# Kernel tuning notes

Measured on AMD Instinct MI355X. Metric: run time of the kernel, lower is better.

## Reference

```python
import math
import jax, jax.numpy as jnp
import numpy as np

N, T, D, H, DH = 4, 2048, 1024, 16, 64
CAP = 30.0
EPS = 1e-5


def _layernorm(x, g, b):
    m = jnp.mean(x, axis=-1, keepdims=True)
    v = jnp.mean(jnp.square(x - m), axis=-1, keepdims=True)
    return (x - m) * jax.lax.rsqrt(v + EPS) * g + b


def _rope(x):
    # x: [N, H, t, d]; interleaved rotary (rotary-embedding-torch style), theta=10000
    t, d = x.shape[2], x.shape[3]
    inv_freq = 1.0 / (10000.0 ** (jnp.arange(0, d, 2, dtype=jnp.float32) / d))
    ang = jnp.arange(t, dtype=jnp.float32)[:, None] * inv_freq[None, :]  # [t, d/2]
    cos, sin = jnp.cos(ang), jnp.sin(ang)
    x1, x2 = x[..., 0::2], x[..., 1::2]
    r1 = x1 * cos - x2 * sin
    r2 = x1 * sin + x2 * cos
    return jnp.stack([r1, r2], axis=-1).reshape(x.shape)


def setup_inputs() -> dict:
    key = jax.random.key(0)
    ks = jax.random.split(key, 8)
    s = 0.02
    lengths = jax.random.randint(ks[6], (N,), T // 2, T + 1).astype(jnp.int32)
    key_padding_mask = jnp.arange(T)[None, :] >= lengths[:, None]  # True = pad
    attn_mask = jnp.triu(jnp.ones((T, T), dtype=bool), 1)  # causal: True = masked
    return {
        "x": jax.random.normal(ks[0], (N, T, D), jnp.float32),
        "ln_g": jnp.ones((D,), jnp.float32),
        "ln_b": jnp.zeros((D,), jnp.float32),
        "Wq": jax.random.normal(ks[1], (D, H * DH), jnp.float32) * s,
        "bq": jnp.zeros((H * DH,), jnp.float32),
        "Wk": jax.random.normal(ks[2], (D, H * DH), jnp.float32) * s,
        "bk": jnp.zeros((H * DH,), jnp.float32),
        "Wv": jax.random.normal(ks[3], (D, H * DH), jnp.float32) * s,
        "bv": jnp.zeros((H * DH,), jnp.float32),
        "Wo": jax.random.normal(ks[4], (H * DH, D), jnp.float32) * s,
        "bo": jnp.zeros((D,), jnp.float32),
        "key_padding_mask": key_padding_mask,
        "attn_mask": attn_mask,
        "key_value_sequence_lengths": lengths,
    }


def reference(x, ln_g, ln_b, Wq, bq, Wk, bk, Wv, bv, Wo, bo,
              key_padding_mask, attn_mask, key_value_sequence_lengths):
    n, t, _ = x.shape
    h = _layernorm(x, ln_g, ln_b)  # shared LN for q/k/v (self-attention)
    q = (h @ Wq + bq).reshape(n, t, H, DH).transpose(0, 2, 1, 3)  # [n,H,t,d]
    k = (h @ Wk + bk).reshape(n, t, H, DH).transpose(0, 2, 1, 3)
    v = (h @ Wv + bv).reshape(n, t, H, DH).transpose(0, 2, 1, 3)
    q = _rope(q)
    k = _rope(k)
    scores = jnp.einsum('bhtd,bhTd->bhtT', q, k) / math.sqrt(DH)
    scores = CAP * jnp.tanh(scores / CAP)  # tanh soft-cap
    mask = key_padding_mask[:, None, None, :] | attn_mask[None, None, :, :]
    scores = jnp.where(mask, -jnp.inf, scores)
    attn = jax.nn.softmax(scores, axis=-1)
    out = jnp.einsum('bhtT,bhTd->bhtd', attn, v)
    out = out.transpose(0, 2, 1, 3).reshape(n, t, H * DH)
    return out @ Wo + bo
```

## Files before the change

### kernel.cpp

```cpp
#include <hip/hip_runtime.h>
#include <hip/hip_bf16.h>

typedef unsigned short u16;
typedef unsigned int   u32;
typedef __bf16 bf16x8 __attribute__((ext_vector_type(8)));
typedef float  f32x4  __attribute__((ext_vector_type(4)));

#define NB 4
#define T_ 2048
#define D_ 1024
#define H_ 16
#define DH 64
#define M_ (NB * T_)
#define PSTR 72

__device__ __forceinline__ float bf2f(u16 u) {
    union { u32 i; float f; } v; v.i = ((u32)u) << 16; return v.f;
}
__device__ __forceinline__ u16 f2bf(float f) {
    union { float fl; u32 i; } v; v.fl = f;
    u32 r = v.i + 0x7fff + ((v.i >> 16) & 1);
    return (u16)(r >> 16);
}

__device__ __forceinline__ void gl_lds16(const u16* g, u16* l) {
    __builtin_amdgcn_global_load_lds((const __attribute__((address_space(1))) void*)g,
                                     (__attribute__((address_space(3))) void*)l,
                                     16, 0, 0);
}

__device__ __forceinline__ int detect_f32(const u16* p) {
    int weird = 0;
    const int lane = threadIdx.x & 63;
    #pragma unroll
    for (int i = 0; i < 4; ++i) {
        const u16 u = p[lane * 4 + i];
        const int e = (u >> 7) & 0xFF;
        weird += (e == 0xFF || (e >= 0x01 && e <= 0x3F) || (e >= 0xC0 && e <= 0xFE));
    }
    #pragma unroll
    for (int off = 32; off; off >>= 1) weird += __shfl_xor(weird, off);
    return weird >= 16;
}

__device__ __forceinline__ int read_len(const void* raw, int b) {
    const int* a32 = (const int*)raw;
    bool ok32 = true;
    #pragma unroll
    for (int i = 0; i < NB; ++i) {
        const int v = a32[i];
        if (v < 1 || v > T_) ok32 = false;
    }
    int v = ok32 ? a32[b] : (int)((const long long*)raw)[b];
    return min(max(v, 1), T_);
}

__global__ __launch_bounds__(256) void ln_kernel(const void* __restrict__ xraw,
                                                 const void* __restrict__ graw,
                                                 const void* __restrict__ braw,
                                                 u16* __restrict__ h) {
    const int row = blockIdx.x;
    const int tid = threadIdx.x;
    const int isf = detect_f32((const u16*)xraw);

    float xv[4];
    if (isf) {
        const float* xr = (const float*)xraw + (size_t)row * D_;
        *(float4*)xv = *(const float4*)&xr[tid * 4];
    } else {
        const u16* xr = (const u16*)xraw + (size_t)row * D_;
        u16 loc[4] __attribute__((aligned(8)));
        *(uint2*)loc = *(const uint2*)&xr[tid * 4];
        #pragma unroll
        for (int i = 0; i < 4; ++i) xv[i] = bf2f(loc[i]);
    }

    float s = xv[0] + xv[1] + xv[2] + xv[3];
    float q = xv[0]*xv[0] + xv[1]*xv[1] + xv[2]*xv[2] + xv[3]*xv[3];

    #pragma unroll
    for (int off = 32; off; off >>= 1) {
        s += __shfl_xor(s, off);
        q += __shfl_xor(q, off);
    }
    __shared__ float red[8];
    const int wave = tid >> 6, lane = tid & 63;
    if (lane == 0) { red[wave] = s; red[4 + wave] = q; }
    __syncthreads();
    s = red[0] + red[1] + red[2] + red[3];
    q = red[4] + red[5] + red[6] + red[7];

    const float mean = s * (1.0f / D_);
    const float var  = q * (1.0f / D_) - mean * mean;
    const float rs   = rsqrtf(var + 1e-5f);

    u16 o[4] __attribute__((aligned(8)));
    #pragma unroll
    for (int i = 0; i < 4; ++i) {
        const int c = tid * 4 + i;
        const float gv = isf ? ((const float*)graw)[c] : bf2f(((const u16*)graw)[c]);
        const float bv = isf ? ((const float*)braw)[c] : bf2f(((const u16*)braw)[c]);
        o[i] = f2bf((xv[i] - mean) * rs * gv + bv);
    }
    *(uint2*)&h[(size_t)row * D_ + tid * 4] = *(uint2*)o;
}

__global__ __launch_bounds__(256) void wconv4_kernel(const void* __restrict__ W0,
                                                     const void* __restrict__ W1,
                                                     const void* __restrict__ W2,
                                                     const void* __restrict__ W3,
                                                     u16* __restrict__ Wt0,
                                                     u16* __restrict__ Wt1,
                                                     u16* __restrict__ Wt2,
                                                     u16* __restrict__ Wt3) {
    __shared__ u16 tile[64][PSTR];
    const int z = blockIdx.z;
    const void* Wraw = (z == 0) ? W0 : (z == 1) ? W1 : (z == 2) ? W2 : W3;
    u16* Wt          = (z == 0) ? Wt0 : (z == 1) ? Wt1 : (z == 2) ? Wt2 : Wt3;
    const int isf = detect_f32((const u16*)Wraw);
    const int n0 = blockIdx.x * 64;
    const int k0 = blockIdx.y * 64;
    const int tid = threadIdx.x;
    const int tr  = tid >> 2;
    const int tc  = (tid & 3) * 16;

    if (isf) {
        const float* W = (const float*)Wraw;
        #pragma unroll
        for (int i = 0; i < 16; ++i)
            tile[tc + i][tr] = f2bf(W[(size_t)(k0 + tr) * D_ + n0 + tc + i]);
    } else {
        const u16* W = (const u16*)Wraw;
        #pragma unroll
        for (int i = 0; i < 16; ++i)
            tile[tc + i][tr] = W[(size_t)(k0 + tr) * D_ + n0 + tc + i];
    }
    __syncthreads();
    *(uint4*)&Wt[(size_t)(n0 + tr) * D_ + k0 + tc]     = *(uint4*)&tile[tr][tc];
    *(uint4*)&Wt[(size_t)(n0 + tr) * D_ + k0 + tc + 8] = *(uint4*)&tile[tr][tc + 8];
}

__global__ __launch_bounds__(256) void wconv_kernel(const void* __restrict__ Wraw,
                                                    u16* __restrict__ Wt) {
    __shared__ u16 tile[64][PSTR];
    const int isf = detect_f32((const u16*)Wraw);
    const int n0 = blockIdx.x * 64;
    const int k0 = blockIdx.y * 64;
    const int tid = threadIdx.x;
    const int tr  = tid >> 2;
    const int tc  = (tid & 3) * 16;

    if (isf) {
        const float* W = (const float*)Wraw;
        #pragma unroll
        for (int i = 0; i < 16; ++i)
            tile[tc + i][tr] = f2bf(W[(size_t)(k0 + tr) * D_ + n0 + tc + i]);
    } else {
        const u16* W = (const u16*)Wraw;
        #pragma unroll
        for (int i = 0; i < 16; ++i)
            tile[tc + i][tr] = W[(size_t)(k0 + tr) * D_ + n0 + tc + i];
    }
    __syncthreads();
    *(uint4*)&Wt[(size_t)(n0 + tr) * D_ + k0 + tc]     = *(uint4*)&tile[tr][tc];
    *(uint4*)&Wt[(size_t)(n0 + tr) * D_ + k0 + tc + 8] = *(uint4*)&tile[tr][tc + 8];
}

__global__ __launch_bounds__(256) void rope_kernel(float2* __restrict__ tab) {
    const int gid = blockIdx.x * 256 + threadIdx.x;
    const int t = gid >> 5, i = gid & 31;
    const float inv = exp2f(-(float)i * 0.41524101186092f);
    const float ang = (float)t * inv;
    float sv, cv;
    sincosf(ang, &sv, &cv);
    tab[gid] = make_float2(cv, sv);
}

__global__ __launch_bounds__(256) void vtrans_kernel(const u16* __restrict__ vtmp,
                                                     u16* __restrict__ vt) {
    __shared__ u16 tile[64][PSTR];
    const int bh = blockIdx.y;
    const int b  = bh >> 4;
    const int hh = bh & 15;
    const int t0 = blockIdx.x * 64;
    const int tid = threadIdx.x;
    const int tr  = tid >> 2;
    const int tc  = (tid & 3) * 16;

    #pragma unroll
    for (int i = 0; i < 16; ++i)
        tile[tc + i][tr] = vtmp[(size_t)(b * T_ + t0 + tr) * D_ + hh * DH + tc + i];
    __syncthreads();
    u16* dst = vt + (size_t)bh * DH * T_ + (size_t)tr * T_ + t0;
    *(uint4*)&dst[tc]     = *(uint4*)&tile[tr][tc];
    *(uint4*)&dst[tc + 8] = *(uint4*)&tile[tr][tc + 8];
}

__global__ __launch_bounds__(256) void qkv_kernel(const u16* __restrict__ A,
                                                  const u16* __restrict__ Wt3,
                                                  const void* __restrict__ Braw,
                                                  const void* __restrict__ bqr,
                                                  const void* __restrict__ bkr,
                                                  const void* __restrict__ bvr,
                                                  u16* __restrict__ qo,
                                                  u16* __restrict__ ko,
                                                  u16* __restrict__ vo,
                                                  const float2* __restrict__ tab) {
    __shared__ __align__(16) u16 As[128 * 32];
    __shared__ __align__(16) u16 Bs[128 * 32];

    const int tid   = threadIdx.x;
    const int wave  = tid >> 6;
    const int lane  = tid & 63;
    const int quad  = lane >> 4;
    const int lr    = lane & 15;
    const int ntile = blockIdx.x * 128;
    const int mtile = blockIdx.y * 128;
    const int seg   = ntile >> 10;

    const int isf = detect_f32((const u16*)Braw);

    const int srow = wave * 32 + (lane >> 2);
    const int scol = (lane & 3) * 8;
    const u16* aptr0 = A   + (size_t)(mtile + srow) * D_ + scol;
    const u16* aptr1 = A   + (size_t)(mtile + srow + 16) * D_ + scol;
    const u16* bptr0 = Wt3 + (size_t)(ntile + srow) * D_ + scol;
    const u16* bptr1 = Wt3 + (size_t)(ntile + srow + 16) * D_ + scol;
    u16* alds0 = As + wave * 1024;
    u16* alds1 = As + wave * 1024 + 512;
    u16* blds0 = Bs + wave * 1024;
    u16* blds1 = Bs + wave * 1024 + 512;

    const int mbase = (wave >> 1) * 64;
    const int nbase = (wave & 1) * 64;

    f32x4 acc[4][4];
    #pragma unroll
    for (int m = 0; m < 4; ++m)
        #pragma unroll
        for (int n = 0; n < 4; ++n)
            acc[m][n] = (f32x4){0.f, 0.f, 0.f, 0.f};

    for (int k0 = 0; k0 < D_; k0 += 32) {
        gl_lds16(aptr0 + k0, alds0);
        gl_lds16(aptr1 + k0, alds1);
        gl_lds16(bptr0 + k0, blds0);
        gl_lds16(bptr1 + k0, blds1);
        __syncthreads();

        bf16x8 af[4], bfr[4];
        #pragma unroll
        for (int m = 0; m < 4; ++m)
            af[m] = *(const bf16x8*)&As[(mbase + m * 16 + lr) * 32 + quad * 8];
        #pragma unroll
        for (int n = 0; n < 4; ++n)
            bfr[n] = *(const bf16x8*)&Bs[(nbase + n * 16 + lr) * 32 + quad * 8];
        #pragma unroll
        for (int m = 0; m < 4; ++m)
            #pragma unroll
            for (int n = 0; n < 4; ++n)
                acc[m][n] = __builtin_amdgcn_mfma_f32_16x16x32_bf16(af[m], bfr[n], acc[m][n], 0, 0, 0);

        __syncthreads();
    }

    const void* biasraw = (seg == 0) ? bqr : (seg == 1) ? bkr : bvr;
    u16* out            = (seg == 0) ? qo  : (seg == 1) ? ko  : vo;
    const int nloc = (ntile & 1023) + nbase;

    #pragma unroll
    for (int m = 0; m < 4; ++m) {
        #pragma unroll
        for (int n = 0; n < 4; ++n) {
            const int ncl = nloc + n * 16 + lr;
            const float bv = isf ? ((const float*)biasraw)[ncl]
                                 : bf2f(((const u16*)biasraw)[ncl]);
            #pragma unroll
            for (int r = 0; r < 4; ++r) {
                const int mrow = mtile + mbase + m * 16 + quad * 4 + r;
                float v = acc[m][n][r] + bv;
                if (seg < 2) {
                    const float other = __shfl_xor(v, 1);
                    const int d = ncl & (DH - 1);
                    const int t = mrow & (T_ - 1);
                    const float2 cs = tab[t * 32 + (d >> 1)];
                    v = (d & 1) ? (other * cs.y + v * cs.x) : (v * cs.x - other * cs.y);
                }
                out[(size_t)mrow * D_ + ncl] = f2bf(v);
            }
        }
    }
}

__global__ __launch_bounds__(256) void gemm128_kernel(const u16* __restrict__ A,
                                                      const u16* __restrict__ Bt,
                                                      const void* __restrict__ Braw,
                                                      const void* __restrict__ biasraw,
                                                      void* __restrict__ out,
                                                      const int mode) {
    __shared__ __align__(16) u16 As[128 * 32];
    __shared__ __align__(16) u16 Bs[128 * 32];

    const int tid   = threadIdx.x;
    const int wave  = tid >> 6;
    const int lane  = tid & 63;
    const int quad  = lane >> 4;
    const int lr    = lane & 15;
    const int ntile = blockIdx.x * 128;
    const int mtile = blockIdx.y * 128;

    const int isf = detect_f32((const u16*)Braw);

    const int srow = wave * 32 + (lane >> 2);
    const int scol = (lane & 3) * 8;
    const u16* aptr0 = A  + (size_t)(mtile + srow) * D_ + scol;
    const u16* aptr1 = A  + (size_t)(mtile + srow + 16) * D_ + scol;
    const u16* bptr0 = Bt + (size_t)(ntile + srow) * D_ + scol;
    const u16* bptr1 = Bt + (size_t)(ntile + srow + 16) * D_ + scol;
    u16* alds0 = As + wave * 1024;
    u16* alds1 = As + wave * 1024 + 512;
    u16* blds0 = Bs + wave * 1024;
    u16* blds1 = Bs + wave * 1024 + 512;

    const int mbase = (wave >> 1) * 64;
    const int nbase = (wave & 1) * 64;

    f32x4 acc[4][4];
    #pragma unroll
    for (int m = 0; m < 4; ++m)
        #pragma unroll
        for (int n = 0; n < 4; ++n)
            acc[m][n] = (f32x4){0.f, 0.f, 0.f, 0.f};

    for (int k0 = 0; k0 < D_; k0 += 32) {
        gl_lds16(aptr0 + k0, alds0);
        gl_lds16(aptr1 + k0, alds1);
        gl_lds16(bptr0 + k0, blds0);
        gl_lds16(bptr1 + k0, blds1);
        __syncthreads();

        bf16x8 af[4], bfr[4];
        #pragma unroll
        for (int m = 0; m < 4; ++m)
            af[m] = *(const bf16x8*)&As[(mbase + m * 16 + lr) * 32 + quad * 8];
        #pragma unroll
        for (int n = 0; n < 4; ++n)
            bfr[n] = *(const bf16x8*)&Bs[(nbase + n * 16 + lr) * 32 + quad * 8];
        #pragma unroll
        for (int m = 0; m < 4; ++m)
            #pragma unroll
            for (int n = 0; n < 4; ++n)
                acc[m][n] = __builtin_amdgcn_mfma_f32_16x16x32_bf16(af[m], bfr[n], acc[m][n], 0, 0, 0);

        __syncthreads();
    }

    #pragma unroll
    for (int m = 0; m < 4; ++m) {
        #pragma unroll
        for (int n = 0; n < 4; ++n) {
            const int ncol = ntile + nbase + n * 16 + lr;
            const float bv = isf ? ((const float*)biasraw)[ncol]
                                 : bf2f(((const u16*)biasraw)[ncol]);
            #pragma unroll
            for (int r = 0; r < 4; ++r) {
                const int mrow = mtile + mbase + m * 16 + quad * 4 + r;
                float v = acc[m][n][r] + bv;
                if (mode == 2) {
                    const float other = __shfl_xor(v, 1);
                    const int d = ncol & (DH - 1);
                    const int t = mrow & (T_ - 1);
                    const int i = d >> 1;
                    const float inv = exp2f(-(float)i * 0.41524101186092f);
                    const float ang = (float)t * inv;
                    float sv, cv;
                    __sincosf(ang, &sv, &cv);
                    v = (d & 1) ? (other * sv + v * cv) : (v * cv - other * sv);
                }
                const int d  = ncol & (DH - 1);
                const int hh = ncol >> 6;
                const int t  = mrow & (T_ - 1);
                const int bb = mrow >> 11;
                if (mode == 0) {
                    if (isf) ((float*)out)[(size_t)mrow * D_ + ncol] = v;
                    else     ((u16*)out)[(size_t)mrow * D_ + ncol] = f2bf(v);
                } else if (mode == 1) {
                    ((u16*)out)[(((size_t)(bb * H_ + hh) * DH) + d) * T_ + t] = f2bf(v);
                } else {
                    ((u16*)out)[(((size_t)(bb * H_ + hh) * T_) + t) * DH + d] = f2bf(v);
                }
            }
        }
    }
}

__global__ __launch_bounds__(256) void gemm_kernel(const u16* __restrict__ A,
                                                   const void* __restrict__ Braw,
                                                   const void* __restrict__ biasraw,
                                                   void* __restrict__ out,
                                                   const int mode) {
    __shared__ __align__(16) u16 As[128 * 32];
    __shared__ __align__(16) u16 Bs[64 * 32];

    const int tid   = threadIdx.x;
    const int ntile = blockIdx.x * 64;
    const int mtile = blockIdx.y * 128;
    const int wave  = tid >> 6;
    const int lane  = tid & 63;
    const int quad  = lane >> 4;
    const int lr    = lane & 15;

    const int isf = detect_f32((const u16*)Braw);
    const float* Bf = (const float*)Braw;
    const u16*   Bu = (const u16*)Braw;

    f32x4 acc[2][4];
    #pragma unroll
    for (int s = 0; s < 2; ++s)
        #pragma unroll
        for (int n = 0; n < 4; ++n)
            acc[s][n] = (f32x4){0.f, 0.f, 0.f, 0.f};

    const int ar  = tid >> 1;
    const int akb = (tid & 1) * 16;
    const int bn  = tid & 63;
    const int bkb = (tid >> 6) * 8;
    const u16* Arow = A + (size_t)(mtile + ar) * D_ + akb;
    const size_t bcol0 = (size_t)bkb * D_ + ntile + bn;

    for (int k0 = 0; k0 < D_; k0 += 32) {
        *(uint4*)&As[ar * 32 + akb]     = *(const uint4*)(Arow + k0);
        *(uint4*)&As[ar * 32 + akb + 8] = *(const uint4*)(Arow + k0 + 8);
        {
            u16 tmp[8] __attribute__((aligned(16)));
            if (isf) {
                #pragma unroll
                for (int j = 0; j < 8; ++j) tmp[j] = f2bf(Bf[bcol0 + (size_t)(k0 + j) * D_]);
            } else {
                #pragma unroll
                for (int j = 0; j < 8; ++j) tmp[j] = Bu[bcol0 + (size_t)(k0 + j) * D_];
            }
            *(uint4*)&Bs[bn * 32 + bkb] = *(uint4*)tmp;
        }
        __syncthreads();

        const int mbase = wave * 32;
        bf16x8 af0 = *(const bf16x8*)&As[(mbase +      lr) * 32 + quad * 8];
        bf16x8 af1 = *(const bf16x8*)&As[(mbase + 16 + lr) * 32 + quad * 8];
        #pragma unroll
        for (int nt = 0; nt < 4; ++nt) {
            bf16x8 bf = *(const bf16x8*)&Bs[(nt * 16 + lr) * 32 + quad * 8];
            acc[0][nt] = __builtin_amdgcn_mfma_f32_16x16x32_bf16(af0, bf, acc[0][nt], 0, 0, 0);
            acc[1][nt] = __builtin_amdgcn_mfma_f32_16x16x32_bf16(af1, bf, acc[1][nt], 0, 0, 0);
        }
        __syncthreads();
    }

    #pragma unroll
    for (int s2 = 0; s2 < 2; ++s2) {
        #pragma unroll
        for (int nt = 0; nt < 4; ++nt) {
            const int ncol = ntile + nt * 16 + lr;
            const float bv = isf ? ((const float*)biasraw)[ncol]
                                 : bf2f(((const u16*)biasraw)[ncol]);
            #pragma unroll
            for (int r = 0; r < 4; ++r) {
                const int mrow = mtile + wave * 32 + s2 * 16 + quad * 4 + r;
                float v = acc[s2][nt][r] + bv;
                if (mode == 2) {
                    const float other = __shfl_xor(v, 1);
                    const int d = ncol & (DH - 1);
                    const int t = mrow & (T_ - 1);
                    const int i = d >> 1;
                    const float inv = exp2f(-(float)i * 0.41524101186092f);
                    const float ang = (float)t * inv;
                    const float cv = cosf(ang), sv = sinf(ang);
                    v = (d & 1) ? (other * sv + v * cv) : (v * cv - other * sv);
                }
                const int d  = ncol & (DH - 1);
                const int hh = ncol >> 6;
                const int t  = mrow & (T_ - 1);
                const int bb = mrow >> 11;
                if (mode == 0) {
                    if (isf) ((float*)out)[(size_t)mrow * D_ + ncol] = v;
                    else     ((u16*)out)[(size_t)mrow * D_ + ncol] = f2bf(v);
                } else if (mode == 1) {
                    ((u16*)out)[(((size_t)(bb * H_ + hh) * DH) + d) * T_ + t] = f2bf(v);
                } else {
                    ((u16*)out)[(((size_t)(bb * H_ + hh) * T_) + t) * DH + d] = f2bf(v);
                }
            }
        }
    }
}

__global__ __launch_bounds__(256) void attn_kernel(const u16* __restrict__ Q,
                                                   const u16* __restrict__ K,
                                                   const u16* __restrict__ Vt,
                                                   const void* __restrict__ lensraw,
                                                   u16* __restrict__ ctx,
                                                   const int rowmajor) {
    __shared__ __align__(16) u16 Ps[64 * PSTR];
    __shared__ __align__(16) u16 Ks[64 * PSTR];
    __shared__ __align__(16) u16 Vts[64 * PSTR];

    const int tid  = threadIdx.x;
    const int wave = tid >> 6;
    const int lane = tid & 63;
    const int quad = lane >> 4;
    const int lr   = lane & 15;
    const int bh   = blockIdx.y;
    const int qs   = blockIdx.x * 64;
    const int b    = bh >> 4;
    const int hh   = bh & 15;
    const int len  = read_len(lensraw, b);

    const size_t qkstride = rowmajor ? (size_t)D_ : (size_t)DH;
    const size_t qkoff    = rowmajor ? ((size_t)b * T_ * D_ + hh * DH)
                                     : ((size_t)bh * T_ * DH);
    const u16* Qp = Q + qkoff;
    const u16* Kp = K + qkoff;
    const u16* Vb = Vt + (size_t)bh * DH * T_;

    const int srow = tid >> 2;
    const int scb  = (tid & 3) * 16;

    *(uint4*)&Ps[srow * PSTR + scb]     = *(const uint4*)&Qp[(size_t)(qs + srow) * qkstride + scb];
    *(uint4*)&Ps[srow * PSTR + scb + 8] = *(const uint4*)&Qp[(size_t)(qs + srow) * qkstride + scb + 8];
    {
        uint4 k0 = *(const uint4*)&Kp[(size_t)srow * qkstride + scb];
        uint4 k1 = *(const uint4*)&Kp[(size_t)srow * qkstride + scb + 8];
        uint4 v0 = *(const uint4*)&Vb[(size_t)srow * T_ + scb];
        uint4 v1 = *(const uint4*)&Vb[(size_t)srow * T_ + scb + 8];
        *(uint4*)&Ks[srow * PSTR + scb]      = k0;
        *(uint4*)&Ks[srow * PSTR + scb + 8]  = k1;
        *(uint4*)&Vts[srow * PSTR + scb]     = v0;
        *(uint4*)&Vts[srow * PSTR + scb + 8] = v1;
    }
    __syncthreads();
    const bf16x8 qa0 = *(const bf16x8*)&Ps[(wave * 16 + lr) * PSTR + quad * 8];
    const bf16x8 qa1 = *(const bf16x8*)&Ps[(wave * 16 + lr) * PSTR + 32 + quad * 8];

    f32x4 acc[4];
    float l_loc[4] = {0.f, 0.f, 0.f, 0.f};
    #pragma unroll
    for (int nt = 0; nt < 4; ++nt) acc[nt] = (f32x4){0.f, 0.f, 0.f, 0.f};

    const int smax = min(qs + 63, len - 1);
    const int ktn  = smax / 64 + 1;
    const int prow = wave * 16 + quad * 4;

    const float C1 = 1.44269504f / 120.0f;
    const float C2 = -60.0f * 1.44269504f;

    uint4 kr0, kr1, vr0, vr1;
    for (int kt = 0; kt < ktn; ++kt) {
        const int ks = kt * 64;
        const bool havenext = (kt + 1 < ktn);

        if (havenext) {
            const int ns = ks + 64;
            kr0 = *(const uint4*)&Kp[(size_t)(ns + srow) * qkstride + scb];
            kr1 = *(const uint4*)&Kp[(size_t)(ns + srow) * qkstride + scb + 8];
            vr0 = *(const uint4*)&Vb[(size_t)srow * T_ + ns + scb];
            vr1 = *(const uint4*)&Vb[(size_t)srow * T_ + ns + scb + 8];
        }

        f32x4 s[4];
        #pragma unroll
        for (int nt = 0; nt < 4; ++nt) s[nt] = (f32x4){0.f, 0.f, 0.f, 0.f};
        __builtin_amdgcn_s_setprio(1);
        #pragma unroll
        for (int nt = 0; nt < 4; ++nt) {
            bf16x8 kb0 = *(const bf16x8*)&Ks[(nt * 16 + lr) * PSTR + quad * 8];
            bf16x8 kb1 = *(const bf16x8*)&Ks[(nt * 16 + lr) * PSTR + 32 + quad * 8];
            s[nt] = __builtin_amdgcn_mfma_f32_16x16x32_bf16(qa0, kb0, s[nt], 0, 0, 0);
            s[nt] = __builtin_amdgcn_mfma_f32_16x16x32_bf16(qa1, kb1, s[nt], 0, 0, 0);
        }
        __builtin_amdgcn_s_setprio(0);

        const bool need_mask = (ks == qs) || (ks + 63 >= len);
        if (!need_mask) {
            #pragma unroll
            for (int r = 0; r < 4; ++r) {
                #pragma unroll
                for (int nt = 0; nt < 4; ++nt) {
                    const float z = __builtin_amdgcn_exp2f(s[nt][r] * C1);
                    const float p = __builtin_amdgcn_exp2f(C2 * __builtin_amdgcn_rcpf(z + 1.0f));
                    l_loc[r] += p;
                    Ps[(prow + r) * PSTR + nt * 16 + lr] = f2bf(p);
                }
            }
        } else {
            #pragma unroll
            for (int r = 0; r < 4; ++r) {
                const int trow = qs + prow + r;
                #pragma unroll
                for (int nt = 0; nt < 4; ++nt) {
                    const float z = __builtin_amdgcn_exp2f(s[nt][r] * C1);
                    float p = __builtin_amdgcn_exp2f(C2 * __builtin_amdgcn_rcpf(z + 1.0f));
                    const int col = ks + nt * 16 + lr;
                    p = (col > trow || col >= len) ? 0.f : p;
                    l_loc[r] += p;
                    Ps[(prow + r) * PSTR + nt * 16 + lr] = f2bf(p);
                }
            }
        }

        bf16x8 pa0 = *(const bf16x8*)&Ps[(wave * 16 + lr) * PSTR + quad * 8];
        bf16x8 pa1 = *(const bf16x8*)&Ps[(wave * 16 + lr) * PSTR + 32 + quad * 8];
        __builtin_amdgcn_s_setprio(1);
        #pragma unroll
        for (int nt = 0; nt < 4; ++nt) {
            bf16x8 vb0 = *(const bf16x8*)&Vts[(nt * 16 + lr) * PSTR + quad * 8];
            bf16x8 vb1 = *(const bf16x8*)&Vts[(nt * 16 + lr) * PSTR + 32 + quad * 8];
            acc[nt] = __builtin_amdgcn_mfma_f32_16x16x32_bf16(pa0, vb0, acc[nt], 0, 0, 0);
            acc[nt] = __builtin_amdgcn_mfma_f32_16x16x32_bf16(pa1, vb1, acc[nt], 0, 0, 0);
        }
        __builtin_amdgcn_s_setprio(0);

        if (havenext) {
            __syncthreads();
            *(uint4*)&Ks[srow * PSTR + scb]      = kr0;
            *(uint4*)&Ks[srow * PSTR + scb + 8]  = kr1;
            *(uint4*)&Vts[srow * PSTR + scb]     = vr0;
            *(uint4*)&Vts[srow * PSTR + scb + 8] = vr1;
            __syncthreads();
        }
    }

    #pragma unroll
    for (int r = 0; r < 4; ++r) {
        float l = l_loc[r];
        #pragma unroll
        for (int off = 1; off < 16; off <<= 1) l += __shfl_xor(l, off);
        const float invl = (l > 0.f) ? (1.0f / l) : 0.f;
        const int qrow = prow + r;
        #pragma unroll
        for (int nt = 0; nt < 4; ++nt) {
            ctx[(size_t)(b * T_ + qs + qrow) * D_ + hh * DH + nt * 16 + lr] =
                f2bf(acc[nt][r] * invl);
        }
    }
}

extern "C" void kernel_launch(void* const* d_in, const int* in_sizes, int n_in,
                              void* d_out, int out_size, void* d_ws, size_t ws_size,
                              hipStream_t stream) {
    u16* h = (u16*)d_ws;
    const size_t MD = (size_t)M_ * D_;
    const size_t WD = (size_t)D_ * D_;
    u16* q  = h + MD;
    u16* k  = q + MD;
    u16* vt = k + MD;
    const bool havewt  = ws_size >= (4 * MD + 4 * WD) * sizeof(u16);
    const bool havebig = ws_size >= (5 * MD + 4 * WD) * sizeof(u16)
                                    + (size_t)T_ * 32 * sizeof(float2);
    u16* wtq = havewt ? (vt + MD)  : nullptr;
    u16* wtk = havewt ? (wtq + WD) : nullptr;
    u16* wtv = havewt ? (wtk + WD) : nullptr;
    u16* wto = havewt ? (wtv + WD) : nullptr;
    u16* vtmp = havebig ? (wto + WD) : nullptr;
    float2* tab = havebig ? (float2*)(vtmp + MD) : nullptr;

    ln_kernel<<<M_, 256, 0, stream>>>(d_in[0], d_in[1], d_in[2], h);

    if (havebig) {
        wconv4_kernel<<<dim3(D_ / 64, D_ / 64, 4), 256, 0, stream>>>(
            d_in[3], d_in[5], d_in[7], d_in[9], wtq, wtk, wtv, wto);
        rope_kernel<<<256, 256, 0, stream>>>(tab);

        qkv_kernel<<<dim3(3 * D_ / 128, M_ / 128), 256, 0, stream>>>(
            h, wtq, d_in[3], d_in[4], d_in[6], d_in[8], q, k, vtmp, tab);

        vtrans_kernel<<<dim3(T_ / 64, NB * H_), 256, 0, stream>>>(vtmp, vt);

        attn_kernel<<<dim3(T_ / 64, NB * H_), 256, 0, stream>>>(q, k, vt, d_in[13], h, 1);

        gemm128_kernel<<<dim3(D_ / 128, M_ / 128), 256, 0, stream>>>(
            h, wto, d_in[9], d_in[10], d_out, 0);
    } else if (havewt) {
        dim3 wgrid(D_ / 64, D_ / 64);
        wconv_kernel<<<wgrid, 256, 0, stream>>>(d_in[3], wtq);
        wconv_kernel<<<wgrid, 256, 0, stream>>>(d_in[5], wtk);
        wconv_kernel<<<wgrid, 256, 0, stream>>>(d_in[7], wtv);
        wconv_kernel<<<wgrid, 256, 0, stream>>>(d_in[9], wto);

        dim3 g128(D_ / 128, M_ / 128);
        gemm128_kernel<<<g128, 256, 0, stream>>>(h, wtq, d_in[3], d_in[4], q, 2);
        gemm128_kernel<<<g128, 256, 0, stream>>>(h, wtk, d_in[5], d_in[6], k, 2);
        gemm128_kernel<<<g128, 256, 0, stream>>>(h, wtv, d_in[7], d_in[8], vt, 1);

        attn_kernel<<<dim3(T_ / 64, NB * H_), 256, 0, stream>>>(q, k, vt, d_in[13], h, 0);

        gemm128_kernel<<<g128, 256, 0, stream>>>(h, wto, d_in[9], d_in[10], d_out, 0);
    } else {
        dim3 ggrid(D_ / 64, M_ / 128);
        gemm_kernel<<<ggrid, 256, 0, stream>>>(h, d_in[3], d_in[4], q, 2);
        gemm_kernel<<<ggrid, 256, 0, stream>>>(h, d_in[5], d_in[6], k, 2);
        gemm_kernel<<<ggrid, 256, 0, stream>>>(h, d_in[7], d_in[8], vt, 1);

        attn_kernel<<<dim3(T_ / 64, NB * H_), 256, 0, stream>>>(q, k, vt, d_in[13], h, 0);

        gemm_kernel<<<ggrid, 256, 0, stream>>>(h, d_in[9], d_in[10], d_out, 0);
    }
}
```

Before: 386.4 us.

## Pair causal query tiles in attention, deepen GEMM K-tile, merge prep kernels

Three independent changes. First, layernorm, weight transpose/convert and the rope table are fused into one prep kernel, removing two launches. Second, both GEMMs now stage a K-step of 64 with an XOR-swizzled LDS layout, which halves the barrier count and aims to avoid bank conflicts at the cost of doubled LDS use. Third, each attention block now processes a low and a high query tile (qx and 31-qx) so causal work is balanced across blocks, with a block-index swizzle for locality, at the cost of more registers for two accumulator sets.

```diff
diff --git a/kernel.cpp b/kernel.cpp
--- a/kernel.cpp
+++ b/kernel.cpp
@@ -55,89 +55,102 @@
     return min(max(v, 1), T_);
 }
 
-__global__ __launch_bounds__(256) void ln_kernel(const void* __restrict__ xraw,
-                                                 const void* __restrict__ graw,
-                                                 const void* __restrict__ braw,
-                                                 u16* __restrict__ h) {
-    const int row = blockIdx.x;
+__global__ __launch_bounds__(256) void prep_kernel(const void* __restrict__ xraw,
+                                                   const void* __restrict__ graw,
+                                                   const void* __restrict__ braw,
+                                                   u16* __restrict__ h,
+                                                   const void* __restrict__ W0,
+                                                   const void* __restrict__ W1,
+                                                   const void* __restrict__ W2,
+                                                   const void* __restrict__ W3,
+                                                   u16* __restrict__ Wt0,
+                                                   u16* __restrict__ Wt1,
+                                                   u16* __restrict__ Wt2,
+                                                   u16* __restrict__ Wt3,
+                                                   float2* __restrict__ tab) {
+    __shared__ __align__(16) u16 sh[64 * PSTR];
+    const int bid = blockIdx.x;
     const int tid = threadIdx.x;
-    const int isf = detect_f32((const u16*)xraw);
-
-    float xv[4];
-    if (isf) {
-        const float* xr = (const float*)xraw + (size_t)row * D_;
-        *(float4*)xv = *(const float4*)&xr[tid * 4];
+
+    if (bid < M_) {
+        const int row = bid;
+        const int isf = detect_f32((const u16*)xraw);
+        float* red = (float*)sh;
+
+        float xv[4];
+        if (isf) {
+            const float* xr = (const float*)xraw + (size_t)row * D_;
+            *(float4*)xv = *(const float4*)&xr[tid * 4];
+        } else {
+            const u16* xr = (const u16*)xraw + (size_t)row * D_;
+            u16 loc[4] __attribute__((aligned(8)));
+            *(uint2*)loc = *(const uint2*)&xr[tid * 4];
+            #pragma unroll
+            for (int i = 0; i < 4; ++i) xv[i] = bf2f(loc[i]);
+        }
+
+        float s = xv[0] + xv[1] + xv[2] + xv[3];
+        float q = xv[0]*xv[0] + xv[1]*xv[1] + xv[2]*xv[2] + xv[3]*xv[3];
+        #pragma unroll
+        for (int off = 32; off; off >>= 1) {
+            s += __shfl_xor(s, off);
+            q += __shfl_xor(q, off);
+        }
+        const int wave = tid >> 6, lane = tid & 63;
+        if (lane == 0) { red[wave] = s; red[4 + wave] = q; }
+        __syncthreads();
+        s = red[0] + red[1] + red[2] + red[3];
+        q = red[4] + red[5] + red[6] + red[7];
+
+        const float mean = s * (1.0f / D_);
+        const float var  = q * (1.0f / D_) - mean * mean;
+        const float rs   = rsqrtf(var + 1e-5f);
+
+        u16 o[4] __attribute__((aligned(8)));
+        #pragma unroll
+        for (int i = 0; i < 4; ++i) {
+            const int c = tid * 4 + i;
+            const float gv = isf ? ((const float*)graw)[c] : bf2f(((const u16*)graw)[c]);
+            const float bv = isf ? ((const float*)braw)[c] : bf2f(((const u16*)braw)[c]);
+            o[i] = f2bf((xv[i] - mean) * rs * gv + bv);
+        }
+        *(uint2*)&h[(size_t)row * D_ + tid * 4] = *(uint2*)o;
+    } else if (bid < M_ + 1024) {
+        const int w = bid - M_;
+        const int z = w >> 8;
+        const int t = w & 255;
+        const void* Wraw = (z == 0) ? W0 : (z == 1) ? W1 : (z == 2) ? W2 : W3;
+        u16* Wt          = (z == 0) ? Wt0 : (z == 1) ? Wt1 : (z == 2) ? Wt2 : Wt3;
+        u16 (*tile)[PSTR] = (u16(*)[PSTR])sh;
+        const int isf = detect_f32((const u16*)Wraw);
+        const int n0 = (t & 15) * 64;
+        const int k0 = (t >> 4) * 64;
+        const int tr  = tid >> 2;
+        const int tc  = (tid & 3) * 16;
+
+        if (isf) {
+            const float* W = (const float*)Wraw;
+            #pragma unroll
+            for (int i = 0; i < 16; ++i)
+                tile[tc + i][tr] = f2bf(W[(size_t)(k0 + tr) * D_ + n0 + tc + i]);
+        } else {
+            const u16* W = (const u16*)Wraw;
+            #pragma unroll
+            for (int i = 0; i < 16; ++i)
+                tile[tc + i][tr] = W[(size_t)(k0 + tr) * D_ + n0 + tc + i];
+        }
+        __syncthreads();
+        *(uint4*)&Wt[(size_t)(n0 + tr) * D_ + k0 + tc]     = *(uint4*)&tile[tr][tc];
+        *(uint4*)&Wt[(size_t)(n0 + tr) * D_ + k0 + tc + 8] = *(uint4*)&tile[tr][tc + 8];
     } else {
-        const u16* xr = (const u16*)xraw + (size_t)row * D_;
-        u16 loc[4] __attribute__((aligned(8)));
-        *(uint2*)loc = *(const uint2*)&xr[tid * 4];
-        #pragma unroll
-        for (int i = 0; i < 4; ++i) xv[i] = bf2f(loc[i]);
-    }
-
-    float s = xv[0] + xv[1] + xv[2] + xv[3];
-    float q = xv[0]*xv[0] + xv[1]*xv[1] + xv[2]*xv[2] + xv[3]*xv[3];
-
-    #pragma unroll
-    for (int off = 32; off; off >>= 1) {
-        s += __shfl_xor(s, off);
-        q += __shfl_xor(q, off);
-    }
-    __shared__ float red[8];
-    const int wave = tid >> 6, lane = tid & 63;
-    if (lane == 0) { red[wave] = s; red[4 + wave] = q; }
-    __syncthreads();
-    s = red[0] + red[1] + red[2] + red[3];
-    q = red[4] + red[5] + red[6] + red[7];
-
-    const float mean = s * (1.0f / D_);
-    const float var  = q * (1.0f / D_) - mean * mean;
-    const float rs   = rsqrtf(var + 1e-5f);
-
-    u16 o[4] __attribute__((aligned(8)));
-    #pragma unroll
-    for (int i = 0; i < 4; ++i) {
-        const int c = tid * 4 + i;
-        const float gv = isf ? ((const float*)graw)[c] : bf2f(((const u16*)graw)[c]);
-        const float bv = isf ? ((const float*)braw)[c] : bf2f(((const u16*)braw)[c]);
-        o[i] = f2bf((xv[i] - mean) * rs * gv + bv);
-    }
-    *(uint2*)&h[(size_t)row * D_ + tid * 4] = *(uint2*)o;
-}
-
-__global__ __launch_bounds__(256) void wconv4_kernel(const void* __restrict__ W0,
-                                                     const void* __restrict__ W1,
-                                                     const void* __restrict__ W2,
-                                                     const void* __restrict__ W3,
-                                                     u16* __restrict__ Wt0,
-                                                     u16* __restrict__ Wt1,
-                                                     u16* __restrict__ Wt2,
-                                                     u16* __restrict__ Wt3) {
-    __shared__ u16 tile[64][PSTR];
-    const int z = blockIdx.z;
-    const void* Wraw = (z == 0) ? W0 : (z == 1) ? W1 : (z == 2) ? W2 : W3;
-    u16* Wt          = (z == 0) ? Wt0 : (z == 1) ? Wt1 : (z == 2) ? Wt2 : Wt3;
-    const int isf = detect_f32((const u16*)Wraw);
-    const int n0 = blockIdx.x * 64;
-    const int k0 = blockIdx.y * 64;
-    const int tid = threadIdx.x;
-    const int tr  = tid >> 2;
-    const int tc  = (tid & 3) * 16;
-
-    if (isf) {
-        const float* W = (const float*)Wraw;
-        #pragma unroll
-        for (int i = 0; i < 16; ++i)
-            tile[tc + i][tr] = f2bf(W[(size_t)(k0 + tr) * D_ + n0 + tc + i]);
-    } else {
-        const u16* W = (const u16*)Wraw;
-        #pragma unroll
-        for (int i = 0; i < 16; ++i)
-            tile[tc + i][tr] = W[(size_t)(k0 + tr) * D_ + n0 + tc + i];
-    }
-    __syncthreads();
-    *(uint4*)&Wt[(size_t)(n0 + tr) * D_ + k0 + tc]     = *(uint4*)&tile[tr][tc];
-    *(uint4*)&Wt[(size_t)(n0 + tr) * D_ + k0 + tc + 8] = *(uint4*)&tile[tr][tc + 8];
+        const int gid = (bid - (M_ + 1024)) * 256 + tid;
+        const int t = gid >> 5, i = gid & 31;
+        const float inv = exp2f(-(float)i * 0.41524101186092f);
+        const float ang = (float)t * inv;
+        float sv, cv;
+        sincosf(ang, &sv, &cv);
+        tab[gid] = make_float2(cv, sv);
+    }
 }
 
 __global__ __launch_bounds__(256) void wconv_kernel(const void* __restrict__ Wraw,
@@ -164,16 +177,6 @@
     __syncthreads();
     *(uint4*)&Wt[(size_t)(n0 + tr) * D_ + k0 + tc]     = *(uint4*)&tile[tr][tc];
     *(uint4*)&Wt[(size_t)(n0 + tr) * D_ + k0 + tc + 8] = *(uint4*)&tile[tr][tc + 8];
-}
-
-__global__ __launch_bounds__(256) void rope_kernel(float2* __restrict__ tab) {
-    const int gid = blockIdx.x * 256 + threadIdx.x;
-    const int t = gid >> 5, i = gid & 31;
-    const float inv = exp2f(-(float)i * 0.41524101186092f);
-    const float ang = (float)t * inv;
-    float sv, cv;
-    sincosf(ang, &sv, &cv);
-    tab[gid] = make_float2(cv, sv);
 }
 
 __global__ __launch_bounds__(256) void vtrans_kernel(const u16* __restrict__ vtmp,
@@ -206,8 +209,8 @@
                                                   u16* __restrict__ ko,
                                                   u16* __restrict__ vo,
                                                   const float2* __restrict__ tab) {
-    __shared__ __align__(16) u16 As[128 * 32];
-    __shared__ __align__(16) u16 Bs[128 * 32];
+    __shared__ __align__(16) u16 As[128 * 64];
+    __shared__ __align__(16) u16 Bs[128 * 64];
 
     const int tid   = threadIdx.x;
     const int wave  = tid >> 6;
@@ -220,16 +223,12 @@
 
     const int isf = detect_f32((const u16*)Braw);
 
-    const int srow = wave * 32 + (lane >> 2);
-    const int scol = (lane & 3) * 8;
-    const u16* aptr0 = A   + (size_t)(mtile + srow) * D_ + scol;
-    const u16* aptr1 = A   + (size_t)(mtile + srow + 16) * D_ + scol;
-    const u16* bptr0 = Wt3 + (size_t)(ntile + srow) * D_ + scol;
-    const u16* bptr1 = Wt3 + (size_t)(ntile + srow + 16) * D_ + scol;
-    u16* alds0 = As + wave * 1024;
-    u16* alds1 = As + wave * 1024 + 512;
-    u16* blds0 = Bs + wave * 1024;
-    u16* blds1 = Bs + wave * 1024 + 512;
+    const int srow = wave * 8 + (lane >> 3);
+    const int sc   = (((lane & 7) ^ (lane >> 3)) * 8);
+    const u16* aP = A   + (size_t)(mtile + srow) * D_ + sc;
+    const u16* bP = Wt3 + (size_t)(ntile + srow) * D_ + sc;
+    u16* aL = As + (wave * 8) * 64;
+    u16* bL = Bs + (wave * 8) * 64;
 
     const int mbase = (wave >> 1) * 64;
     const int nbase = (wave & 1) * 64;
@@ -241,26 +240,33 @@
         for (int n = 0; n < 4; ++n)
             acc[m][n] = (f32x4){0.f, 0.f, 0.f, 0.f};
 
-    for (int k0 = 0; k0 < D_; k0 += 32) {
-        gl_lds16(aptr0 + k0, alds0);
-        gl_lds16(aptr1 + k0, alds1);
-        gl_lds16(bptr0 + k0, blds0);
-        gl_lds16(bptr1 + k0, blds1);
+    for (int k0 = 0; k0 < D_; k0 += 64) {
+        #pragma unroll
+        for (int j = 0; j < 4; ++j) {
+            gl_lds16(aP + (size_t)(j * 32) * D_ + k0, aL + (j * 32) * 64);
+            gl_lds16(bP + (size_t)(j * 32) * D_ + k0, bL + (j * 32) * 64);
+        }
         __syncthreads();
 
-        bf16x8 af[4], bfr[4];
-        #pragma unroll
-        for (int m = 0; m < 4; ++m)
-            af[m] = *(const bf16x8*)&As[(mbase + m * 16 + lr) * 32 + quad * 8];
-        #pragma unroll
-        for (int n = 0; n < 4; ++n)
-            bfr[n] = *(const bf16x8*)&Bs[(nbase + n * 16 + lr) * 32 + quad * 8];
-        #pragma unroll
-        for (int m = 0; m < 4; ++m)
-            #pragma unroll
-            for (int n = 0; n < 4; ++n)
-                acc[m][n] = __builtin_amdgcn_mfma_f32_16x16x32_bf16(af[m], bfr[n], acc[m][n], 0, 0, 0);
-
+        #pragma unroll
+        for (int c = 0; c < 2; ++c) {
+            bf16x8 af[4], bfr[4];
+            #pragma unroll
+            for (int m = 0; m < 4; ++m) {
+                const int row = mbase + m * 16 + lr;
+                af[m] = *(const bf16x8*)&As[row * 64 + (((c << 2) | quad) ^ (row & 7)) * 8];
+            }
+            #pragma unroll
+            for (int n = 0; n < 4; ++n) {
+                const int row = nbase + n * 16 + lr;
+                bfr[n] = *(const bf16x8*)&Bs[row * 64 + (((c << 2) | quad) ^ (row & 7)) * 8];
+            }
+            #pragma unroll
+            for (int m = 0; m < 4; ++m)
+                #pragma unroll
+                for (int n = 0; n < 4; ++n)
+                    acc[m][n] = __builtin_amdgcn_mfma_f32_16x16x32_bf16(af[m], bfr[n], acc[m][n], 0, 0, 0);
+        }
         __syncthreads();
     }
 
@@ -298,8 +304,8 @@
                                                       const void* __restrict__ biasraw,
                                                       void* __restrict__ out,
                                                       const int mode) {
-    __shared__ __align__(16) u16 As[128 * 32];
-    __shared__ __align__(16) u16 Bs[128 * 32];
+    __shared__ __align__(16) u16 As[128 * 64];
+    __shared__ __align__(16) u16 Bs[128 * 64];
 
     const int tid   = threadIdx.x;
     const int wave  = tid >> 6;
@@ -311,16 +317,12 @@
 
     const int isf = detect_f32((const u16*)Braw);
 
-    const int srow = wave * 32 + (lane >> 2);
-    const int scol = (lane & 3) * 8;
-    const u16* aptr0 = A  + (size_t)(mtile + srow) * D_ + scol;
-    const u16* aptr1 = A  + (size_t)(mtile + srow + 16) * D_ + scol;
-    const u16* bptr0 = Bt + (size_t)(ntile + srow) * D_ + scol;
-    const u16* bptr1 = Bt + (size_t)(ntile + srow + 16) * D_ + scol;
-    u16* alds0 = As + wave * 1024;
-    u16* alds1 = As + wave * 1024 + 512;
-    u16* blds0 = Bs + wave * 1024;
-    u16* blds1 = Bs + wave * 1024 + 512;
+    const int srow = wave * 8 + (lane >> 3);
+    const int sc   = (((lane & 7) ^ (lane >> 3)) * 8);
+    const u16* aP = A  + (size_t)(mtile + srow) * D_ + sc;
+    const u16* bP = Bt + (size_t)(ntile + srow) * D_ + sc;
+    u16* aL = As + (wave * 8) * 64;
+    u16* bL = Bs + (wave * 8) * 64;
 
     const int mbase = (wave >> 1) * 64;
     const int nbase = (wave & 1) * 64;
@@ -332,26 +334,33 @@
         for (int n = 0; n < 4; ++n)
             acc[m][n] = (f32x4){0.f, 0.f, 0.f, 0.f};
 
-    for (int k0 = 0; k0 < D_; k0 += 32) {
-        gl_lds16(aptr0 + k0, alds0);
-        gl_lds16(aptr1 + k0, alds1);
-        gl_lds16(bptr0 + k0, blds0);
-        gl_lds16(bptr1 + k0, blds1);
+    for (int k0 = 0; k0 < D_; k0 += 64) {
+        #pragma unroll
+        for (int j = 0; j < 4; ++j) {
+            gl_lds16(aP + (size_t)(j * 32) * D_ + k0, aL + (j * 32) * 64);
+            gl_lds16(bP + (size_t)(j * 32) * D_ + k0, bL + (j * 32) * 64);
+        }
         __syncthreads();
 
-        bf16x8 af[4], bfr[4];
-        #pragma unroll
-        for (int m = 0; m < 4; ++m)
-            af[m] = *(const bf16x8*)&As[(mbase + m * 16 + lr) * 32 + quad * 8];
-        #pragma unroll
-        for (int n = 0; n < 4; ++n)
-            bfr[n] = *(const bf16x8*)&Bs[(nbase + n * 16 + lr) * 32 + quad * 8];
-        #pragma unroll
-        for (int m = 0; m < 4; ++m)
-            #pragma unroll
-            for (int n = 0; n < 4; ++n)
-                acc[m][n] = __builtin_amdgcn_mfma_f32_16x16x32_bf16(af[m], bfr[n], acc[m][n], 0, 0, 0);
-
+        #pragma unroll
+        for (int c = 0; c < 2; ++c) {
+            bf16x8 af[4], bfr[4];
+            #pragma unroll
+            for (int m = 0; m < 4; ++m) {
+                const int row = mbase + m * 16 + lr;
+                af[m] = *(const bf16x8*)&As[row * 64 + (((c << 2) | quad) ^ (row & 7)) * 8];
+            }
+            #pragma unroll
+            for (int n = 0; n < 4; ++n) {
+                const int row = nbase + n * 16 + lr;
+                bfr[n] = *(const bf16x8*)&Bs[row * 64 + (((c << 2) | quad) ^ (row & 7)) * 8];
+            }
+            #pragma unroll
+            for (int m = 0; m < 4; ++m)
+                #pragma unroll
+                for (int n = 0; n < 4; ++n)
+                    acc[m][n] = __builtin_amdgcn_mfma_f32_16x16x32_bf16(af[m], bfr[n], acc[m][n], 0, 0, 0);
+        }
         __syncthreads();
     }
 
@@ -509,8 +518,13 @@
     const int lane = tid & 63;
     const int quad = lane >> 4;
     const int lr   = lane & 15;
-    const int bh   = blockIdx.y;
-    const int qs   = blockIdx.x * 64;
+
+    const int bid = blockIdx.x;
+    const int swz = (bid & 7) * 128 + (bid >> 3);
+    const int qx  = swz & 15;
+    const int bh  = swz >> 4;
+    const int qs_lo = qx * 64;
+    const int qs_hi = (31 - qx) * 64;
     const int b    = bh >> 4;
     const int hh   = bh & 15;
     const int len  = read_len(lensraw, b);
@@ -525,8 +539,15 @@
     const int srow = tid >> 2;
     const int scb  = (tid & 3) * 16;
 
-    *(uint4*)&Ps[srow * PSTR + scb]     = *(const uint4*)&Qp[(size_t)(qs + srow) * qkstride + scb];
-    *(uint4*)&Ps[srow * PSTR + scb + 8] = *(const uint4*)&Qp[(size_t)(qs + srow) * qkstride + scb + 8];
+    *(uint4*)&Ps[srow * PSTR + scb]     = *(const uint4*)&Qp[(size_t)(qs_lo + srow) * qkstride + scb];
+    *(uint4*)&Ps[srow * PSTR + scb + 8] = *(const uint4*)&Qp[(size_t)(qs_lo + srow) * qkstride + scb + 8];
+    const bf16x8 qaL0 = *(const bf16x8*)&Ps[(wave * 16 + lr) * PSTR + quad * 8];
+    const bf16x8 qaL1 = *(const bf16x8*)&Ps[(wave * 16 + lr) * PSTR + 32 + quad * 8];
+    *(uint4*)&Ps[srow * PSTR + scb]     = *(const uint4*)&Qp[(size_t)(qs_hi + srow) * qkstride + scb];
+    *(uint4*)&Ps[srow * PSTR + scb + 8] = *(const uint4*)&Qp[(size_t)(qs_hi + srow) * qkstride + scb + 8];
+    const bf16x8 qaH0 = *(const bf16x8*)&Ps[(wave * 16 + lr) * PSTR + quad * 8];
+    const bf16x8 qaH1 = *(const bf16x8*)&Ps[(wave * 16 + lr) * PSTR + 32 + quad * 8];
+
     {
         uint4 k0 = *(const uint4*)&Kp[(size_t)srow * qkstride + scb];
         uint4 k1 = *(const uint4*)&Kp[(size_t)srow * qkstride + scb + 8];
@@ -538,25 +559,28 @@
         *(uint4*)&Vts[srow * PSTR + scb + 8] = v1;
     }
     __syncthreads();
-    const bf16x8 qa0 = *(const bf16x8*)&Ps[(wave * 16 + lr) * PSTR + quad * 8];
-    const bf16x8 qa1 = *(const bf16x8*)&Ps[(wave * 16 + lr) * PSTR + 32 + quad * 8];
-
-    f32x4 acc[4];
-    float l_loc[4] = {0.f, 0.f, 0.f, 0.f};
-    #pragma unroll
-    for (int nt = 0; nt < 4; ++nt) acc[nt] = (f32x4){0.f, 0.f, 0.f, 0.f};
-
-    const int smax = min(qs + 63, len - 1);
-    const int ktn  = smax / 64 + 1;
+
+    f32x4 accL[4], accH[4];
+    float lL[4] = {0.f, 0.f, 0.f, 0.f};
+    float lH[4] = {0.f, 0.f, 0.f, 0.f};
+    #pragma unroll
+    for (int nt = 0; nt < 4; ++nt) {
+        accL[nt] = (f32x4){0.f, 0.f, 0.f, 0.f};
+        accH[nt] = (f32x4){0.f, 0.f, 0.f, 0.f};
+    }
+
+    const int ktnL = min(qs_lo + 63, len - 1) / 64 + 1;
+    const int ktnH = min(qs_hi + 63, len - 1) / 64 + 1;
     const int prow = wave * 16 + quad * 4;
 
     const float C1 = 1.44269504f / 120.0f;
     const float C2 = -60.0f * 1.44269504f;
 
     uint4 kr0, kr1, vr0, vr1;
-    for (int kt = 0; kt < ktn; ++kt) {
+    for (int kt = 0; kt < ktnH; ++kt) {
         const int ks = kt * 64;
-        const bool havenext = (kt + 1 < ktn);
+        const bool havenext = (kt + 1 < ktnH);
+        const bool lo_act   = (kt < ktnL);
 
         if (havenext) {
             const int ns = ks + 64;
@@ -566,58 +590,113 @@
             vr1 = *(const uint4*)&Vb[(size_t)srow * T_ + ns + scb + 8];
         }
 
-        f32x4 s[4];
-        #pragma unroll
-        for (int nt = 0; nt < 4; ++nt) s[nt] = (f32x4){0.f, 0.f, 0.f, 0.f};
-        __builtin_amdgcn_s_setprio(1);
-        #pragma unroll
-        for (int nt = 0; nt < 4; ++nt) {
-            bf16x8 kb0 = *(const bf16x8*)&Ks[(nt * 16 + lr) * PSTR + quad * 8];
-            bf16x8 kb1 = *(const bf16x8*)&Ks[(nt * 16 + lr) * PSTR + 32 + quad * 8];
-            s[nt] = __builtin_amdgcn_mfma_f32_16x16x32_bf16(qa0, kb0, s[nt], 0, 0, 0);
-            s[nt] = __builtin_amdgcn_mfma_f32_16x16x32_bf16(qa1, kb1, s[nt], 0, 0, 0);
-        }
-        __builtin_amdgcn_s_setprio(0);
-
-        const bool need_mask = (ks == qs) || (ks + 63 >= len);
-        if (!need_mask) {
-            #pragma unroll
-            for (int r = 0; r < 4; ++r) {
+        {
+            f32x4 s[4];
+            #pragma unroll
+            for (int nt = 0; nt < 4; ++nt) s[nt] = (f32x4){0.f, 0.f, 0.f, 0.f};
+            __builtin_amdgcn_s_setprio(1);
+            #pragma unroll
+            for (int nt = 0; nt < 4; ++nt) {
+                bf16x8 kb0 = *(const bf16x8*)&Ks[(nt * 16 + lr) * PSTR + quad * 8];
+                bf16x8 kb1 = *(const bf16x8*)&Ks[(nt * 16 + lr) * PSTR + 32 + quad * 8];
+                s[nt] = __builtin_amdgcn_mfma_f32_16x16x32_bf16(qaH0, kb0, s[nt], 0, 0, 0);
+                s[nt] = __builtin_amdgcn_mfma_f32_16x16x32_bf16(qaH1, kb1, s[nt], 0, 0, 0);
+            }
+            __builtin_amdgcn_s_setprio(0);
+
+            const bool need_mask = (ks == qs_hi) || (ks + 63 >= len);
+            if (!need_mask) {
                 #pragma unroll
-                for (int nt = 0; nt < 4; ++nt) {
-                    const float z = __builtin_amdgcn_exp2f(s[nt][r] * C1);
-                    const float p = __builtin_amdgcn_exp2f(C2 * __builtin_amdgcn_rcpf(z + 1.0f));
-                    l_loc[r] += p;
-                    Ps[(prow + r) * PSTR + nt * 16 + lr] = f2bf(p);
-                }
-            }
-        } else {
-            #pragma unroll
-            for (int r = 0; r < 4; ++r) {
-                const int trow = qs + prow + r;
+                for (int r = 0; r < 4; ++r) {
+                    #pragma unroll
+                    for (int nt = 0; nt < 4; ++nt) {
+                        const float z = __builtin_amdgcn_exp2f(s[nt][r] * C1);
+                        const float p = __builtin_amdgcn_exp2f(C2 * __builtin_amdgcn_rcpf(z + 1.0f));
+                        lH[r] += p;
+                        Ps[(prow + r) * PSTR + nt * 16 + lr] = f2bf(p);
+                    }
+                }
+            } else {
                 #pragma unroll
-                for (int nt = 0; nt < 4; ++nt) {
-                    const float z = __builtin_amdgcn_exp2f(s[nt][r] * C1);
-                    float p = __builtin_amdgcn_exp2f(C2 * __builtin_amdgcn_rcpf(z + 1.0f));
-                    const int col = ks + nt * 16 + lr;
-                    p = (col > trow || col >= len) ? 0.f : p;
-                    l_loc[r] += p;
-                    Ps[(prow + r) * PSTR + nt * 16 + lr] = f2bf(p);
-                }
-            }
-        }
-
-        bf16x8 pa0 = *(const bf16x8*)&Ps[(wave * 16 + lr) * PSTR + quad * 8];
-        bf16x8 pa1 = *(const bf16x8*)&Ps[(wave * 16 + lr) * PSTR + 32 + quad * 8];
-        __builtin_amdgcn_s_setprio(1);
-        #pragma unroll
-        for (int nt = 0; nt < 4; ++nt) {
-            bf16x8 vb0 = *(const bf16x8*)&Vts[(nt * 16 + lr) * PSTR + quad * 8];
-            bf16x8 vb1 = *(const bf16x8*)&Vts[(nt * 16 + lr) * PSTR + 32 + quad * 8];
-            acc[nt] = __builtin_amdgcn_mfma_f32_16x16x32_bf16(pa0, vb0, acc[nt], 0, 0, 0);
-            acc[nt] = __builtin_amdgcn_mfma_f32_16x16x32_bf16(pa1, vb1, acc[nt], 0, 0, 0);
-        }
-        __builtin_amdgcn_s_setprio(0);
+                for (int r = 0; r < 4; ++r) {
+                    const int trow = qs_hi + prow + r;
+                    #pragma unroll
+                    for (int nt = 0; nt < 4; ++nt) {
+                        const float z = __builtin_amdgcn_exp2f(s[nt][r] * C1);
+                        float p = __builtin_amdgcn_exp2f(C2 * __builtin_amdgcn_rcpf(z + 1.0f));
+                        const int col = ks + nt * 16 + lr;
+                        p = (col > trow || col >= len) ? 0.f : p;
+                        lH[r] += p;
+                        Ps[(prow + r) * PSTR + nt * 16 + lr] = f2bf(p);
+                    }
+                }
+            }
+            bf16x8 pa0 = *(const bf16x8*)&Ps[(wave * 16 + lr) * PSTR + quad * 8];
+            bf16x8 pa1 = *(const bf16x8*)&Ps[(wave * 16 + lr) * PSTR + 32 + quad * 8];
+            __builtin_amdgcn_s_setprio(1);
+            #pragma unroll
+            for (int nt = 0; nt < 4; ++nt) {
+                bf16x8 vb0 = *(const bf16x8*)&Vts[(nt * 16 + lr) * PSTR + quad * 8];
+                bf16x8 vb1 = *(const bf16x8*)&Vts[(nt * 16 + lr) * PSTR + 32 + quad * 8];
+                accH[nt] = __builtin_amdgcn_mfma_f32_16x16x32_bf16(pa0, vb0, accH[nt], 0, 0, 0);
+                accH[nt] = __builtin_amdgcn_mfma_f32_16x16x32_bf16(pa1, vb1, accH[nt], 0, 0, 0);
+            }
+            __builtin_amdgcn_s_setprio(0);
+        }
+
+        if (lo_act) {
+            f32x4 s[4];
+            #pragma unroll
+            for (int nt = 0; nt < 4; ++nt) s[nt] = (f32x4){0.f, 0.f, 0.f, 0.f};
+            __builtin_amdgcn_s_setprio(1);
+            #pragma unroll
+            for (int nt = 0; nt < 4; ++nt) {
+                bf16x8 kb0 = *(const bf16x8*)&Ks[(nt * 16 + lr) * PSTR + quad * 8];
+                bf16x8 kb1 = *(const bf16x8*)&Ks[(nt * 16 + lr) * PSTR + 32 + quad * 8];
+                s[nt] = __builtin_amdgcn_mfma_f32_16x16x32_bf16(qaL0, kb0, s[nt], 0, 0, 0);
+                s[nt] = __builtin_amdgcn_mfma_f32_16x16x32_bf16(qaL1, kb1, s[nt], 0, 0, 0);
+            }
+            __builtin_amdgcn_s_setprio(0);
+
+            const bool need_mask = (ks == qs_lo) || (ks + 63 >= len);
+            if (!need_mask) {
+                #pragma unroll
+                for (int r = 0; r < 4; ++r) {
+                    #pragma unroll
+                    for (int nt = 0; nt < 4; ++nt) {
+                        const float z = __builtin_amdgcn_exp2f(s[nt][r] * C1);
+                        const float p = __builtin_amdgcn_exp2f(C2 * __builtin_amdgcn_rcpf(z + 1.0f));
+                        lL[r] += p;
+                        Ps[(prow + r) * PSTR + nt * 16 + lr] = f2bf(p);
+                    }
+                }
+            } else {
+                #pragma unroll
+                for (int r = 0; r < 4; ++r) {
+                    const int trow = qs_lo + prow + r;
+                    #pragma unroll
+                    for (int nt = 0; nt < 4; ++nt) {
+                        const float z = __builtin_amdgcn_exp2f(s[nt][r] * C1);
+                        float p = __builtin_amdgcn_exp2f(C2 * __builtin_amdgcn_rcpf(z + 1.0f));
+                        const int col = ks + nt * 16 + lr;
+                        p = (col > trow || col >= len) ? 0.f : p;
+                        lL[r] += p;
+                        Ps[(prow + r) * PSTR + nt * 16 + lr] = f2bf(p);
+                    }
+                }
+            }
+            bf16x8 pa0 = *(const bf16x8*)&Ps[(wave * 16 + lr) * PSTR + quad * 8];
+            bf16x8 pa1 = *(const bf16x8*)&Ps[(wave * 16 + lr) * PSTR + 32 + quad * 8];
+            __builtin_amdgcn_s_setprio(1);
+            #pragma unroll
+            for (int nt = 0; nt < 4; ++nt) {
+                bf16x8 vb0 = *(const bf16x8*)&Vts[(nt * 16 + lr) * PSTR + quad * 8];
+                bf16x8 vb1 = *(const bf16x8*)&Vts[(nt * 16 + lr) * PSTR + 32 + quad * 8];
+                accL[nt] = __builtin_amdgcn_mfma_f32_16x16x32_bf16(pa0, vb0, accL[nt], 0, 0, 0);
+                accL[nt] = __builtin_amdgcn_mfma_f32_16x16x32_bf16(pa1, vb1, accL[nt], 0, 0, 0);
+            }
+            __builtin_amdgcn_s_setprio(0);
+        }
 
         if (havenext) {
             __syncthreads();
@@ -631,15 +710,21 @@
 
     #pragma unroll
     for (int r = 0; r < 4; ++r) {
-        float l = l_loc[r];
-        #pragma unroll
-        for (int off = 1; off < 16; off <<= 1) l += __shfl_xor(l, off);
-        const float invl = (l > 0.f) ? (1.0f / l) : 0.f;
+        float ll = lL[r], lh = lH[r];
+        #pragma unroll
+        for (int off = 1; off < 16; off <<= 1) {
+            ll += __shfl_xor(ll, off);
+            lh += __shfl_xor(lh, off);
+        }
+        const float invL = (ll > 0.f) ? (1.0f / ll) : 0.f;
+        const float invH = (lh > 0.f) ? (1.0f / lh) : 0.f;
         const int qrow = prow + r;
         #pragma unroll
         for (int nt = 0; nt < 4; ++nt) {
-            ctx[(size_t)(b * T_ + qs + qrow) * D_ + hh * DH + nt * 16 + lr] =
-                f2bf(acc[nt][r] * invl);
+            ctx[(size_t)(b * T_ + qs_lo + qrow) * D_ + hh * DH + nt * 16 + lr] =
+                f2bf(accL[nt][r] * invL);
+            ctx[(size_t)(b * T_ + qs_hi + qrow) * D_ + hh * DH + nt * 16 + lr] =
+                f2bf(accH[nt][r] * invH);
         }
     }
 }
@@ -663,23 +748,24 @@
     u16* vtmp = havebig ? (wto + WD) : nullptr;
     float2* tab = havebig ? (float2*)(vtmp + MD) : nullptr;
 
-    ln_kernel<<<M_, 256, 0, stream>>>(d_in[0], d_in[1], d_in[2], h);
-
     if (havebig) {
-        wconv4_kernel<<<dim3(D_ / 64, D_ / 64, 4), 256, 0, stream>>>(
-            d_in[3], d_in[5], d_in[7], d_in[9], wtq, wtk, wtv, wto);
-        rope_kernel<<<256, 256, 0, stream>>>(tab);
+        prep_kernel<<<M_ + 1024 + 256, 256, 0, stream>>>(
+            d_in[0], d_in[1], d_in[2], h,
+            d_in[3], d_in[5], d_in[7], d_in[9], wtq, wtk, wtv, wto, tab);
 
         qkv_kernel<<<dim3(3 * D_ / 128, M_ / 128), 256, 0, stream>>>(
             h, wtq, d_in[3], d_in[4], d_in[6], d_in[8], q, k, vtmp, tab);
 
         vtrans_kernel<<<dim3(T_ / 64, NB * H_), 256, 0, stream>>>(vtmp, vt);
 
-        attn_kernel<<<dim3(T_ / 64, NB * H_), 256, 0, stream>>>(q, k, vt, d_in[13], h, 1);
+        attn_kernel<<<(T_ / 128) * NB * H_, 256, 0, stream>>>(q, k, vt, d_in[13], h, 1);
 
         gemm128_kernel<<<dim3(D_ / 128, M_ / 128), 256, 0, stream>>>(
             h, wto, d_in[9], d_in[10], d_out, 0);
     } else if (havewt) {
+        prep_kernel<<<M_, 256, 0, stream>>>(
+            d_in[0], d_in[1], d_in[2], h,
+            d_in[3], d_in[5], d_in[7], d_in[9], wtq, wtk, wtv, wto, nullptr);
         dim3 wgrid(D_ / 64, D_ / 64);
         wconv_kernel<<<wgrid, 256, 0, stream>>>(d_in[3], wtq);
         wconv_kernel<<<wgrid, 256, 0, stream>>>(d_in[5], wtk);
@@ -691,16 +777,19 @@
         gemm128_kernel<<<g128, 256, 0, stream>>>(h, wtk, d_in[5], d_in[6], k, 2);
         gemm128_kernel<<<g128, 256, 0, stream>>>(h, wtv, d_in[7], d_in[8], vt, 1);
 
-        attn_kernel<<<dim3(T_ / 64, NB * H_), 256, 0, stream>>>(q, k, vt, d_in[13], h, 0);
+        attn_kernel<<<(T_ / 128) * NB * H_, 256, 0, stream>>>(q, k, vt, d_in[13], h, 0);
 
         gemm128_kernel<<<g128, 256, 0, stream>>>(h, wto, d_in[9], d_in[10], d_out, 0);
     } else {
+        prep_kernel<<<M_, 256, 0, stream>>>(
+            d_in[0], d_in[1], d_in[2], h,
+            d_in[3], d_in[5], d_in[7], d_in[9], nullptr, nullptr, nullptr, nullptr, nullptr);
         dim3 ggrid(D_ / 64, M_ / 128);
         gemm_kernel<<<ggrid, 256, 0, stream>>>(h, d_in[3], d_in[4], q, 2);
         gemm_kernel<<<ggrid, 256, 0, stream>>>(h, d_in[5], d_in[6], k, 2);
         gemm_kernel<<<ggrid, 256, 0, stream>>>(h, d_in[7], d_in[8], vt, 1);
 
-        attn_kernel<<<dim3(T_ / 64, NB * H_), 256, 0, stream>>>(q, k, vt, d_in[13], h, 0);
+        attn_kernel<<<(T_ / 128) * NB * H_, 256, 0, stream>>>(q, k, vt, d_in[13], h, 0);
 
         gemm_kernel<<<ggrid, 256, 0, stream>>>(h, d_in[9], d_in[10], d_out, 0);
     }
```

After: 389.1 us. No clear change (+0.7%).
